# Kernel tuning notes

Hardware: AMD Instinct MI355X
Metric: run time of the kernel (lower is better)

Reference implementation:

```python
import jax, jax.numpy as jnp
import numpy as np

K = 3  # number of nearest neighbors
EPS = 1e-10


def setup_inputs() -> dict:
    key = jax.random.key(0)
    k1, k2, k3 = jax.random.split(key, 3)
    B, C, N = 2, 3, 8192
    xyz1 = jax.random.normal(k1, (B, C, N), dtype=jnp.float32)
    xyz2 = jax.random.normal(k2, (B, C, N), dtype=jnp.float32)
    flow1 = jax.random.normal(k3, (B, C, N), dtype=jnp.float32) * 0.1
    return {"xyz1": xyz1, "xyz2": xyz2, "flow1": flow1}


def _square_distance(src, dst):
    # src: [B, N, 3], dst: [B, M, 3] -> [B, N, M]
    d = -2.0 * jnp.einsum('bnc,bmc->bnm', src, dst)
    d = d + jnp.sum(src ** 2, axis=-1)[:, :, None]
    d = d + jnp.sum(dst ** 2, axis=-1)[:, None, :]
    return d


def _gather_group(points, idx):
    # points: [B, N, C], idx: [B, S, K] -> [B, S, K, C]
    return jax.vmap(lambda p, i: p[i])(points, idx)


def reference(xyz1, xyz2, flow1):
    B, C, N1 = xyz1.shape
    N2 = xyz2.shape[2]
    xyz1_to_2 = (xyz1 + flow1).transpose(0, 2, 1)  # [B, N1, 3]
    xyz2_t = xyz2.transpose(0, 2, 1)               # [B, N2, 3]
    flow1_t = flow1.transpose(0, 2, 1)             # [B, N1, 3]

    sqrdists = _square_distance(xyz2_t, xyz1_to_2)  # [B, N2, N1]
    _, knn_idx = jax.lax.top_k(-sqrdists, K)        # smallest K -> [B, N2, K]

    grouped_xyz = _gather_group(xyz1_to_2, knn_idx)           # [B, N2, K, 3]
    diff = grouped_xyz - xyz2_t[:, :, None, :]                 # [B, N2, K, 3]
    dist = jnp.maximum(jnp.linalg.norm(diff, axis=3), EPS)     # [B, N2, K]
    inv = 1.0 / dist
    weight = inv / jnp.sum(inv, axis=2, keepdims=True)         # [B, N2, K]

    grouped_flow = _gather_group(flow1_t, knn_idx)             # [B, N2, K, 3]
    flow2 = jnp.sum(weight[..., None] * grouped_flow, axis=2)  # [B, N2, 3]
    warped_xyz2 = (xyz2_t - flow2).transpose(0, 2, 1)          # [B, 3, N2]
    return warped_xyz2
```

## Files before the change

kernel.cpp:

```cpp
#include <hip/hip_runtime.h>


#define NPTS   8192
#define TILE   2048
#define NTILES (NPTS / TILE)
#define BLOCK  256
#define GROUP  64
#define Q      4
#define QPB    ((BLOCK / GROUP) * Q)
#define KMASK  0xFFFFFF80
#define EPSV   1e-10f

__device__ __forceinline__ void insert3_idx(float k, int idx,
                                            float& m0, float& m1, float& m2,
                                            int& j0, int& j1, int& j2) {
    const bool c0 = k < m0;
    const bool c1 = k < m1;
    const bool c2 = k < m2;
    m2 = __builtin_amdgcn_fmed3f(k, m1, m2);
    m1 = __builtin_amdgcn_fmed3f(k, m0, m1);
    m0 = fminf(k, m0);
    j2 = c1 ? j1 : (c2 ? idx : j2);
    j1 = c0 ? j0 : (c1 ? idx : j1);
    j0 = c0 ? idx : j0;
}

__global__ __launch_bounds__(BLOCK, 4)
void pointwarp_kernel(const float* __restrict__ xyz1,
                      const float* __restrict__ xyz2,
                      const float* __restrict__ flow1,
                      float* __restrict__ out) {
    __shared__ float2 s_xy[TILE];
    __shared__ float  s_z[TILE];

    const int tid = threadIdx.x;
    const int w   = tid >> 6;
    const int t   = tid & 63;
    const int blocksPerB = NPTS / QPB;
    const int b     = blockIdx.x / blocksPerB;
    const int qblk  = (blockIdx.x % blocksPerB) * QPB;
    const int qbase = qblk + w * Q;

    const float* x1 = xyz1 + (size_t)b * 3 * NPTS;
    const float* x2 = xyz2 + (size_t)b * 3 * NPTS;
    const float* f1 = flow1 + (size_t)b * 3 * NPTS;

    float qx[Q], qy[Q], qz[Q], k0[Q], k1[Q], k2[Q];
    #pragma unroll
    for (int i = 0; i < Q; ++i) {
        qx[i] = x2[0*NPTS + qbase + i];
        qy[i] = x2[1*NPTS + qbase + i];
        qz[i] = x2[2*NPTS + qbase + i];
        k0[i] = k1[i] = k2[i] = 3e38f;
    }

    for (int tile = 0; tile < NTILES; ++tile) {
        const int base = tile * TILE;
        for (int j = tid; j < TILE; j += BLOCK) {
            const int n1 = base + j;
            const float px = x1[0*NPTS + n1] + f1[0*NPTS + n1];
            const float py = x1[1*NPTS + n1] + f1[1*NPTS + n1];
            const float pz = x1[2*NPTS + n1] + f1[2*NPTS + n1];
            s_xy[j] = make_float2(px, py);
            s_z[j]  = pz;
        }
        __syncthreads();

        #pragma unroll 4
        for (int j = 0; j < TILE/GROUP; ++j) {
            const int jj = j * GROUP + t;
            const int jg = tile * (TILE/GROUP) + j;
            const float2 pxy = s_xy[jj];
            const float  pz  = s_z[jj];
            #pragma unroll
            for (int i = 0; i < Q; ++i) {
                const float dx = pxy.x - qx[i];
                const float dy = pxy.y - qy[i];
                const float dz = pz    - qz[i];
                const float d  = fmaf(dx, dx, fmaf(dy, dy, dz*dz));
                const float k  = __int_as_float((__float_as_int(d) & KMASK) | jg);
                k2[i] = __builtin_amdgcn_fmed3f(k, k1[i], k2[i]);
                k1[i] = __builtin_amdgcn_fmed3f(k, k0[i], k1[i]);
                k0[i] = fminf(k, k0[i]);
            }
        }
        __syncthreads();
    }

    int i0[Q], i1[Q], i2[Q];
    #pragma unroll
    for (int i = 0; i < Q; ++i) {
        i0[i] = ((__float_as_int(k0[i]) & 0x7F) << 6) | t;
        i1[i] = ((__float_as_int(k1[i]) & 0x7F) << 6) | t;
        i2[i] = ((__float_as_int(k2[i]) & 0x7F) << 6) | t;
    }

    #pragma unroll
    for (int step = 1; step < 64; step <<= 1) {
        #pragma unroll
        for (int i = 0; i < Q; ++i) {
            const float b0 = __shfl_xor(k0[i], step, 64);
            const float b1 = __shfl_xor(k1[i], step, 64);
            const float b2 = __shfl_xor(k2[i], step, 64);
            const int   a0 = __shfl_xor(i0[i], step, 64);
            const int   a1 = __shfl_xor(i1[i], step, 64);
            const int   a2 = __shfl_xor(i2[i], step, 64);
            insert3_idx(b0, a0, k0[i], k1[i], k2[i], i0[i], i1[i], i2[i]);
            insert3_idx(b1, a1, k0[i], k1[i], k2[i], i0[i], i1[i], i2[i]);
            insert3_idx(b2, a2, k0[i], k1[i], k2[i], i0[i], i1[i], i2[i]);
        }
    }

    if (t < Q) {
        #pragma unroll
        for (int i = 0; i < Q; ++i) {
            if (t == i) {
                const int n2 = qbase + i;
                const int j0 = i0[i], j1 = i1[i], j2 = i2[i];
                float dd[3];
                const int js[3] = {j0, j1, j2};
                #pragma unroll
                for (int s = 0; s < 3; ++s) {
                    const int jn = js[s];
                    const float px = x1[0*NPTS + jn] + f1[0*NPTS + jn];
                    const float py = x1[1*NPTS + jn] + f1[1*NPTS + jn];
                    const float pz = x1[2*NPTS + jn] + f1[2*NPTS + jn];
                    const float dx = px - qx[i], dy = py - qy[i], dz = pz - qz[i];
                    dd[s] = fmaf(dx, dx, fmaf(dy, dy, dz*dz));
                }
                float w0 = 1.0f / fmaxf(sqrtf(dd[0]), EPSV);
                float w1 = 1.0f / fmaxf(sqrtf(dd[1]), EPSV);
                float w2 = 1.0f / fmaxf(sqrtf(dd[2]), EPSV);
                const float ws = w0 + w1 + w2;
                w0 /= ws; w1 /= ws; w2 /= ws;

                float* o = out + (size_t)b * 3 * NPTS;
                #pragma unroll
                for (int c = 0; c < 3; ++c) {
                    const float fl = w0 * f1[c*NPTS + j0]
                                   + w1 * f1[c*NPTS + j1]
                                   + w2 * f1[c*NPTS + j2];
                    o[c*NPTS + n2] = x2[c*NPTS + n2] - fl;
                }
            }
        }
    }
}

extern "C" void kernel_launch(void* const* d_in, const int* in_sizes, int n_in,
                              void* d_out, int out_size, void* d_ws, size_t ws_size,
                              hipStream_t stream) {
    const float* xyz1  = (const float*)d_in[0];
    const float* xyz2  = (const float*)d_in[1];
    const float* flow1 = (const float*)d_in[2];
    float* out = (float*)d_out;

    const int B = in_sizes[0] / (3 * NPTS);
    const int grid = B * (NPTS / QPB);
    pointwarp_kernel<<<grid, BLOCK, 0, stream>>>(xyz1, xyz2, flow1, out);
}
```

Measured before the change: 112.6 us.

## Precompute warped candidates into workspace and split candidate scan across wave pairs

Adds a prepass kernel that computes xyz1+flow1 once into a float4 workspace. The main kernel then reads candidates straight from global or L2 instead of staging tiles in shared memory with barriers. Each pair of waves splits the 8192 candidates in half for the same 4 queries, and the two partial top-3 lists are merged through shared memory. This removes per-block recomputation and the tile syncs and doubles the number of blocks. In exchange it adds a second launch, a merge step and global-memory streaming of the candidates.

After: 104.2 us. 1.08x faster.

```diff
diff --git a/kernel.cpp b/kernel.cpp
--- a/kernel.cpp
+++ b/kernel.cpp
@@ -2,14 +2,16 @@
 
 
 #define NPTS   8192
-#define TILE   2048
-#define NTILES (NPTS / TILE)
 #define BLOCK  256
-#define GROUP  64
 #define Q      4
-#define QPB    ((BLOCK / GROUP) * Q)
+#define QPB    8
+#define HALF   4096
 #define KMASK  0xFFFFFF80
 #define EPSV   1e-10f
+
+__device__ __forceinline__ float rfl_f32(float x) {
+    return __int_as_float(__builtin_amdgcn_readfirstlane(__float_as_int(x)));
+}
 
 __device__ __forceinline__ void insert3_idx(float k, int idx,
                                             float& m0, float& m1, float& m2,
@@ -25,66 +27,69 @@
     j0 = c0 ? idx : j0;
 }
 
-__global__ __launch_bounds__(BLOCK, 4)
-void pointwarp_kernel(const float* __restrict__ xyz1,
+__global__ __launch_bounds__(256)
+void warp_points_kernel(const float* __restrict__ xyz1,
+                        const float* __restrict__ flow1,
+                        float4* __restrict__ ws, int total) {
+    const int i = blockIdx.x * 256 + threadIdx.x;
+    if (i >= total) return;
+    const int b = i / NPTS, n = i - b * NPTS;
+    const float* x1 = xyz1 + (size_t)b * 3 * NPTS;
+    const float* f1 = flow1 + (size_t)b * 3 * NPTS;
+    const float px = x1[0*NPTS + n] + f1[0*NPTS + n];
+    const float py = x1[1*NPTS + n] + f1[1*NPTS + n];
+    const float pz = x1[2*NPTS + n] + f1[2*NPTS + n];
+    ws[i] = make_float4(px, py, pz, 0.0f);
+}
+
+__global__ __launch_bounds__(BLOCK, 8)
+void pointwarp_kernel(const float4* __restrict__ wsp,
                       const float* __restrict__ xyz2,
                       const float* __restrict__ flow1,
                       float* __restrict__ out) {
-    __shared__ float2 s_xy[TILE];
-    __shared__ float  s_z[TILE];
+    __shared__ float s_k[2][2][Q][3];
+    __shared__ int   s_i[2][2][Q][3];
 
-    const int tid = threadIdx.x;
-    const int w   = tid >> 6;
-    const int t   = tid & 63;
+    const int tid  = threadIdx.x;
+    const int w    = tid >> 6;
+    const int t    = tid & 63;
+    const int pair = w >> 1;
+    const int w2   = w & 1;
     const int blocksPerB = NPTS / QPB;
     const int b     = blockIdx.x / blocksPerB;
     const int qblk  = (blockIdx.x % blocksPerB) * QPB;
-    const int qbase = qblk + w * Q;
+    const int qbase = qblk + pair * Q;
 
-    const float* x1 = xyz1 + (size_t)b * 3 * NPTS;
-    const float* x2 = xyz2 + (size_t)b * 3 * NPTS;
-    const float* f1 = flow1 + (size_t)b * 3 * NPTS;
+    const float4* cand = wsp + (size_t)b * NPTS;
+    const float*  x2   = xyz2 + (size_t)b * 3 * NPTS;
+    const float*  f1   = flow1 + (size_t)b * 3 * NPTS;
 
     float qx[Q], qy[Q], qz[Q], k0[Q], k1[Q], k2[Q];
     #pragma unroll
     for (int i = 0; i < Q; ++i) {
-        qx[i] = x2[0*NPTS + qbase + i];
-        qy[i] = x2[1*NPTS + qbase + i];
-        qz[i] = x2[2*NPTS + qbase + i];
+        qx[i] = rfl_f32(x2[0*NPTS + qbase + i]);
+        qy[i] = rfl_f32(x2[1*NPTS + qbase + i]);
+        qz[i] = rfl_f32(x2[2*NPTS + qbase + i]);
         k0[i] = k1[i] = k2[i] = 3e38f;
     }
 
-    for (int tile = 0; tile < NTILES; ++tile) {
-        const int base = tile * TILE;
-        for (int j = tid; j < TILE; j += BLOCK) {
-            const int n1 = base + j;
-            const float px = x1[0*NPTS + n1] + f1[0*NPTS + n1];
-            const float py = x1[1*NPTS + n1] + f1[1*NPTS + n1];
-            const float pz = x1[2*NPTS + n1] + f1[2*NPTS + n1];
-            s_xy[j] = make_float2(px, py);
-            s_z[j]  = pz;
+    const float4* base = cand + w2 * HALF + t;
+    const int rowbase = w2 * (HALF / 64);
+    #pragma unroll 4
+    for (int j = 0; j < HALF / 64; ++j) {
+        const float4 p = base[j * 64];
+        const int jg = rowbase + j;
+        #pragma unroll
+        for (int i = 0; i < Q; ++i) {
+            const float dx = p.x - qx[i];
+            const float dy = p.y - qy[i];
+            const float dz = p.z - qz[i];
+            const float d  = fmaf(dx, dx, fmaf(dy, dy, dz*dz));
+            const float k  = __int_as_float((__float_as_int(d) & KMASK) | jg);
+            k2[i] = __builtin_amdgcn_fmed3f(k, k1[i], k2[i]);
+            k1[i] = __builtin_amdgcn_fmed3f(k, k0[i], k1[i]);
+            k0[i] = fminf(k, k0[i]);
         }
-        __syncthreads();
-
-        #pragma unroll 4
-        for (int j = 0; j < TILE/GROUP; ++j) {
-            const int jj = j * GROUP + t;
-            const int jg = tile * (TILE/GROUP) + j;
-            const float2 pxy = s_xy[jj];
-            const float  pz  = s_z[jj];
-            #pragma unroll
-            for (int i = 0; i < Q; ++i) {
-                const float dx = pxy.x - qx[i];
-                const float dy = pxy.y - qy[i];
-                const float dz = pz    - qz[i];
-                const float d  = fmaf(dx, dx, fmaf(dy, dy, dz*dz));
-                const float k  = __int_as_float((__float_as_int(d) & KMASK) | jg);
-                k2[i] = __builtin_amdgcn_fmed3f(k, k1[i], k2[i]);
-                k1[i] = __builtin_amdgcn_fmed3f(k, k0[i], k1[i]);
-                k0[i] = fminf(k, k0[i]);
-            }
-        }
-        __syncthreads();
     }
 
     int i0[Q], i1[Q], i2[Q];
@@ -111,38 +116,54 @@
         }
     }
 
-    if (t < Q) {
+    #pragma unroll
+    for (int i = 0; i < Q; ++i) {
+        if (t == i) {
+            s_k[pair][w2][i][0] = k0[i]; s_i[pair][w2][i][0] = i0[i];
+            s_k[pair][w2][i][1] = k1[i]; s_i[pair][w2][i][1] = i1[i];
+            s_k[pair][w2][i][2] = k2[i]; s_i[pair][w2][i][2] = i2[i];
+        }
+    }
+    __syncthreads();
+
+    if (tid < QPB) {
+        const int u  = tid;
+        const int pr = u >> 2, qi = u & 3;
+        float m0 = 3e38f, m1 = 3e38f, m2 = 3e38f;
+        int   j0 = 0, j1 = 0, j2 = 0;
         #pragma unroll
-        for (int i = 0; i < Q; ++i) {
-            if (t == i) {
-                const int n2 = qbase + i;
-                const int j0 = i0[i], j1 = i1[i], j2 = i2[i];
-                float dd[3];
-                const int js[3] = {j0, j1, j2};
-                #pragma unroll
-                for (int s = 0; s < 3; ++s) {
-                    const int jn = js[s];
-                    const float px = x1[0*NPTS + jn] + f1[0*NPTS + jn];
-                    const float py = x1[1*NPTS + jn] + f1[1*NPTS + jn];
-                    const float pz = x1[2*NPTS + jn] + f1[2*NPTS + jn];
-                    const float dx = px - qx[i], dy = py - qy[i], dz = pz - qz[i];
-                    dd[s] = fmaf(dx, dx, fmaf(dy, dy, dz*dz));
-                }
-                float w0 = 1.0f / fmaxf(sqrtf(dd[0]), EPSV);
-                float w1 = 1.0f / fmaxf(sqrtf(dd[1]), EPSV);
-                float w2 = 1.0f / fmaxf(sqrtf(dd[2]), EPSV);
-                const float ws = w0 + w1 + w2;
-                w0 /= ws; w1 /= ws; w2 /= ws;
+        for (int wv = 0; wv < 2; ++wv) {
+            #pragma unroll
+            for (int s = 0; s < 3; ++s) {
+                insert3_idx(s_k[pr][wv][qi][s], s_i[pr][wv][qi][s],
+                            m0, m1, m2, j0, j1, j2);
+            }
+        }
+        const int n2 = qblk + u;
+        const float gx = x2[0*NPTS + n2];
+        const float gy = x2[1*NPTS + n2];
+        const float gz = x2[2*NPTS + n2];
+        float dd[3];
+        const int js[3] = {j0, j1, j2};
+        #pragma unroll
+        for (int s = 0; s < 3; ++s) {
+            const float4 p = cand[js[s]];
+            const float dx = p.x - gx, dy = p.y - gy, dz = p.z - gz;
+            dd[s] = fmaf(dx, dx, fmaf(dy, dy, dz*dz));
+        }
+        float w0 = 1.0f / fmaxf(sqrtf(dd[0]), EPSV);
+        float w1 = 1.0f / fmaxf(sqrtf(dd[1]), EPSV);
+        float w2v = 1.0f / fmaxf(sqrtf(dd[2]), EPSV);
+        const float ws = w0 + w1 + w2v;
+        w0 /= ws; w1 /= ws; w2v /= ws;
 
-                float* o = out + (size_t)b * 3 * NPTS;
-                #pragma unroll
-                for (int c = 0; c < 3; ++c) {
-                    const float fl = w0 * f1[c*NPTS + j0]
-                                   + w1 * f1[c*NPTS + j1]
-                                   + w2 * f1[c*NPTS + j2];
-                    o[c*NPTS + n2] = x2[c*NPTS + n2] - fl;
-                }
-            }
+        float* o = out + (size_t)b * 3 * NPTS;
+        #pragma unroll
+        for (int c = 0; c < 3; ++c) {
+            const float fl = w0  * f1[c*NPTS + j0]
+                           + w1  * f1[c*NPTS + j1]
+                           + w2v * f1[c*NPTS + j2];
+            o[c*NPTS + n2] = x2[c*NPTS + n2] - fl;
         }
     }
 }
@@ -154,8 +175,11 @@
     const float* xyz2  = (const float*)d_in[1];
     const float* flow1 = (const float*)d_in[2];
     float* out = (float*)d_out;
+    float4* ws = (float4*)d_ws;
 
     const int B = in_sizes[0] / (3 * NPTS);
+    const int total = B * NPTS;
+    warp_points_kernel<<<(total + 255) / 256, 256, 0, stream>>>(xyz1, flow1, ws, total);
     const int grid = B * (NPTS / QPB);
-    pointwarp_kernel<<<grid, BLOCK, 0, stream>>>(xyz1, xyz2, flow1, out);
+    pointwarp_kernel<<<grid, BLOCK, 0, stream>>>(ws, xyz2, flow1, out);
 }
```
